# Kernel tuning notes

Hardware: AMD Instinct MI355X
Metric: run time of the kernel (lower is better)

## Reference

```python
import jax, jax.numpy as jnp
import numpy as np

S1, S2 = 8, 8          # support_size per hub
N, F, B = 100000, 128, 2048
EDGE_DIM = 1


def setup_inputs() -> dict:
    key = jax.random.key(0)
    ks = jax.random.split(key, 6)
    return {
        "features": jax.random.normal(ks[0], (N, F), dtype=jnp.float32),
        "in_sample_amnt": jax.random.uniform(ks[1], (N, S1, EDGE_DIM), dtype=jnp.float32),
        "out_sample_amnt": jax.random.uniform(ks[2], (N, S1, EDGE_DIM), dtype=jnp.float32),
        "in_sample": jax.random.randint(ks[3], (N, S1), 0, N),
        "out_sample": jax.random.randint(ks[4], (N, S1), 0, N),
        "node_ids": jax.random.randint(ks[5], (B,), 0, N),
    }


def _hop(features, sample, amnt, node_ids, support):
    """One hop of __get_next_hub: gather sampled neighbor ids, their edge
    weights, and [edge_weight || node_features] per neighbor."""
    nxt = sample[node_ids][..., :support]              # [..., support] int ids
    w = amnt[node_ids][..., :support, :]               # [..., support, EDGE_DIM]
    f = jnp.concatenate([w, features[nxt]], axis=-1)   # [..., support, EDGE_DIM+F]
    return nxt, f, w[..., 0]                           # squeeze first weight channel


def _branch(features, samples, amnts, node_ids, direction):
    """Hub-1 gather in `direction`, then hub-2 gathers in both directions,
    combined exactly as __get_input_layer does at hub == len(support_size)."""
    nn1, f1, w1 = _hop(features, samples[direction], amnts[direction], node_ids, S1)
    f1 = f1[..., None, :]                              # [B,S1,1,1+F]
    w1 = w1[..., None]                                 # [B,S1,1]
    _, f2i, w2i = _hop(features, samples["in"], amnts["in"], nn1, S2)    # [B,S1,S2,1+F]
    _, f2o, w2o = _hop(features, samples["out"], amnts["out"], nn1, S2)
    # concat([feat, next_in_feat, feat, next_out_feat], -2)
    feat = jnp.concatenate([f1, f2i, f1, f2o], axis=-2)  # [B,S1,2+2*S2,1+F]
    # weight loop collapses to one level (hub-1 weight has a single channel):
    # head = factor**2, deeper weights multiplied by the hub-1 factor.
    head = w1 ** 2
    wc = jnp.concatenate([head, w2i * w1, head, w2o * w1], axis=-1)  # [B,S1,2+2*S2]
    b = feat.shape[0]
    m = S1 * (2 + 2 * S2)
    return feat.reshape(b, m, feat.shape[-1]), wc.reshape(b, m)


def reference(features, in_sample_amnt, out_sample_amnt, in_sample, out_sample, node_ids):
    samples = {"in": in_sample, "out": out_sample}
    amnts = {"in": in_sample_amnt, "out": out_sample_amnt}
    fi, wi = _branch(features, samples, amnts, node_ids, "in")
    fo, wo = _branch(features, samples, amnts, node_ids, "out")
    feat = jnp.concatenate([fi, fo], axis=1)           # [B, 2*S1*(2+2*S2), 1+F]
    weight = jnp.concatenate([wi, wo], axis=1)         # [B, 2*S1*(2+2*S2)]
    # pack (feat, weight) into a single tensor: last channel is the weight
    return jnp.concatenate([feat, weight[..., None]], axis=-1)
```

## Files before the change

### kernel.cpp

```cpp
#include <hip/hip_runtime.h>

constexpr int S1 = 8, S2 = 8, F = 128;
constexpr int ROWS_PER_BRANCH = S1 * (2 + 2 * S2);
constexpr int ROWS_PER_B = 2 * ROWS_PER_BRANCH;
constexpr int ROW_LEN = F + 2;
constexpr int TOTAL_ROWS = 2048 * ROWS_PER_B;
constexpr int SLOTS = ROW_LEN / 2;
constexpr unsigned TOTAL_THREADS = 9360u * 256u;
constexpr int SLOTS_PER_THREAD = 16;

typedef float f32x2 __attribute__((ext_vector_type(2)));
typedef unsigned int u32;

__global__ __launch_bounds__(256) void gae_meta(
    const float* __restrict__ in_amnt,
    const float* __restrict__ out_amnt,
    const int*   __restrict__ in_sample,
    const int*   __restrict__ out_sample,
    const int*   __restrict__ node_ids,
    int4*        __restrict__ meta)
{
    const int row = blockIdx.x * blockDim.x + threadIdx.x;
    const int b  = row / ROWS_PER_B;
    const int r  = row - b * ROWS_PER_B;
    const int d1 = r / ROWS_PER_BRANCH;
    const int rr = r - d1 * ROWS_PER_BRANCH;
    const int s1 = rr / 18;
    const int lr = rr - s1 * 18;

    const int   nid = node_ids[b];
    const int   e1  = nid * S1 + s1;
    const int   n1  = d1 ? out_sample[e1] : in_sample[e1];
    const float w1  = d1 ? out_amnt[e1]   : in_amnt[e1];

    int node; float wf, wt;
    if (lr == 0 || lr == 9) {
        node = n1; wf = w1; wt = w1 * w1;
    } else if (lr <= 8) {
        const int e2 = n1 * S2 + (lr - 1);
        const float w2 = in_amnt[e2];
        node = in_sample[e2]; wf = w2; wt = w2 * w1;
    } else {
        const int e2 = n1 * S2 + (lr - 10);
        const float w2 = out_amnt[e2];
        node = out_sample[e2]; wf = w2; wt = w2 * w1;
    }

    int4 m;
    m.x = node;
    m.y = __float_as_int(wf);
    m.z = __float_as_int(wt);
    m.w = 0;
    meta[row] = m;
}

__global__ __launch_bounds__(256) void gae_scatter(
    const float* __restrict__ features,
    const int4*  __restrict__ meta,
    float*       __restrict__ out)
{
    const u32 tid = blockIdx.x * blockDim.x + threadIdx.x;
    f32x2* __restrict__ out2 = (f32x2*)out;

    #pragma unroll 4
    for (int k = 0; k < SLOTS_PER_THREAD; ++k) {
        const u32 s   = tid + (u32)k * TOTAL_THREADS;
        const u32 row = s / 65u;
        const u32 j   = s - row * 65u;

        const int4  m    = meta[row];
        const float wf   = __int_as_float(m.y);
        const float wt   = __int_as_float(m.z);
        const float* __restrict__ frow = features + (size_t)m.x * F;

        const u32 iA = (j == 0u)  ? 0u   : (2u * j - 1u);
        const u32 iB = (j >= 64u) ? 127u : (2u * j);
        const float a  = frow[iA];
        const float bv = frow[iB];

        f32x2 v;
        v.x = (j == 0u)  ? wf : a;
        v.y = (j == 64u) ? wt : bv;
        __builtin_nontemporal_store(v, &out2[s]);
    }
}

extern "C" void kernel_launch(void* const* d_in, const int* in_sizes, int n_in,
                              void* d_out, int out_size, void* d_ws, size_t ws_size,
                              hipStream_t stream) {
    const float* features   = (const float*)d_in[0];
    const float* in_amnt    = (const float*)d_in[1];
    const float* out_amnt   = (const float*)d_in[2];
    const int*   in_sample  = (const int*)d_in[3];
    const int*   out_sample = (const int*)d_in[4];
    const int*   node_ids   = (const int*)d_in[5];
    float*       out        = (float*)d_out;
    int4*        meta       = (int4*)d_ws;

    gae_meta<<<TOTAL_ROWS / 256, 256, 0, stream>>>(in_amnt, out_amnt,
                                                   in_sample, out_sample,
                                                   node_ids, meta);
    gae_scatter<<<9360, 256, 0, stream>>>(features, meta, out);
}
```

Measured before the change: 102.6 us.

## Sort output rows by source node via counting sort to improve gather locality

Adds a counting sort of output rows keyed by gathered node id: atomic histogram in the meta kernel, a three-kernel prefix scan, and a placement kernel that builds a row order. The scatter kernel then walks rows in node-sorted order, so rows that gather the same feature row run close together in time and should hit in cache. In exchange it adds five extra launches, a memset, global atomics, and output stores that are no longer contiguous across consecutive threads.

```diff
diff --git a/kernel.cpp b/kernel.cpp
--- a/kernel.cpp
+++ b/kernel.cpp
@@ -3,14 +3,20 @@
 constexpr int S1 = 8, S2 = 8, F = 128;
 constexpr int ROWS_PER_BRANCH = S1 * (2 + 2 * S2);
 constexpr int ROWS_PER_B = 2 * ROWS_PER_BRANCH;
-constexpr int ROW_LEN = F + 2;
 constexpr int TOTAL_ROWS = 2048 * ROWS_PER_B;
-constexpr int SLOTS = ROW_LEN / 2;
+constexpr int NNODES = 100000;
+constexpr int SCAN_BLK = 1024;
+constexpr int NBLK = (NNODES + SCAN_BLK - 1) / SCAN_BLK;
 constexpr unsigned TOTAL_THREADS = 9360u * 256u;
 constexpr int SLOTS_PER_THREAD = 16;
 
 typedef float f32x2 __attribute__((ext_vector_type(2)));
 typedef unsigned int u32;
+
+constexpr size_t OFF_NODEA = 9437184;
+constexpr size_t OFF_ORDER = 11796480;
+constexpr size_t OFF_BINS  = 14155776;
+constexpr size_t OFF_BSUM  = 14555776;
 
 __global__ __launch_bounds__(256) void gae_meta(
     const float* __restrict__ in_amnt,
@@ -18,7 +24,7 @@
     const int*   __restrict__ in_sample,
     const int*   __restrict__ out_sample,
     const int*   __restrict__ node_ids,
-    int4*        __restrict__ meta)
+    int4* __restrict__ meta, u32* __restrict__ nodeA, u32* __restrict__ bins)
 {
     const int row = blockIdx.x * blockDim.x + threadIdx.x;
     const int b  = row / ROWS_PER_B;
@@ -46,17 +52,60 @@
         node = out_sample[e2]; wf = w2; wt = w2 * w1;
     }
 
-    int4 m;
-    m.x = node;
-    m.y = __float_as_int(wf);
-    m.z = __float_as_int(wt);
-    m.w = 0;
-    meta[row] = m;
+    int4 m; m.x = node; m.y = __float_as_int(wf); m.z = __float_as_int(wt); m.w = 0;
+    meta[row]  = m;
+    nodeA[row] = (u32)node;
+    atomicAdd(&bins[node], 1u);
+}
+
+__global__ __launch_bounds__(SCAN_BLK) void scan1(u32* __restrict__ bins,
+                                                  u32* __restrict__ bsum)
+{
+    __shared__ u32 tmp[SCAN_BLK];
+    const int t = threadIdx.x;
+    const int i = blockIdx.x * SCAN_BLK + t;
+    const u32 c = (i < NNODES) ? bins[i] : 0u;
+    tmp[t] = c;
+    __syncthreads();
+    for (int off = 1; off < SCAN_BLK; off <<= 1) {
+        const u32 v = tmp[t];
+        const u32 a = (t >= off) ? tmp[t - off] : 0u;
+        __syncthreads();
+        tmp[t] = v + a;
+        __syncthreads();
+    }
+    if (i < NNODES) bins[i] = tmp[t] - c;
+    if (t == SCAN_BLK - 1) bsum[blockIdx.x] = tmp[t];
+}
+
+__global__ void scan2(u32* __restrict__ bsum)
+{
+    if (threadIdx.x == 0 && blockIdx.x == 0) {
+        u32 run = 0;
+        for (int b = 0; b < NBLK; ++b) { const u32 v = bsum[b]; bsum[b] = run; run += v; }
+    }
+}
+
+__global__ __launch_bounds__(SCAN_BLK) void scan3(u32* __restrict__ bins,
+                                                  const u32* __restrict__ bsum)
+{
+    const int i = blockIdx.x * SCAN_BLK + threadIdx.x;
+    if (i < NNODES) bins[i] += bsum[blockIdx.x];
+}
+
+__global__ __launch_bounds__(256) void gae_place(
+    const u32* __restrict__ nodeA, u32* __restrict__ bins, u32* __restrict__ order)
+{
+    const int row = blockIdx.x * blockDim.x + threadIdx.x;
+    const u32 node = nodeA[row];
+    const u32 pos  = atomicAdd(&bins[node], 1u);
+    order[pos] = (u32)row;
 }
 
 __global__ __launch_bounds__(256) void gae_scatter(
     const float* __restrict__ features,
     const int4*  __restrict__ meta,
+    const u32*   __restrict__ order,
     float*       __restrict__ out)
 {
     const u32 tid = blockIdx.x * blockDim.x + threadIdx.x;
@@ -65,12 +114,13 @@
     #pragma unroll 4
     for (int k = 0; k < SLOTS_PER_THREAD; ++k) {
         const u32 s   = tid + (u32)k * TOTAL_THREADS;
-        const u32 row = s / 65u;
-        const u32 j   = s - row * 65u;
+        const u32 kk  = s / 65u;
+        const u32 j   = s - kk * 65u;
+        const u32 row = order[kk];
 
-        const int4  m    = meta[row];
-        const float wf   = __int_as_float(m.y);
-        const float wt   = __int_as_float(m.z);
+        const int4  m  = meta[row];
+        const float wf = __int_as_float(m.y);
+        const float wt = __int_as_float(m.z);
         const float* __restrict__ frow = features + (size_t)m.x * F;
 
         const u32 iA = (j == 0u)  ? 0u   : (2u * j - 1u);
@@ -81,7 +131,7 @@
         f32x2 v;
         v.x = (j == 0u)  ? wf : a;
         v.y = (j == 64u) ? wt : bv;
-        __builtin_nontemporal_store(v, &out2[s]);
+        __builtin_nontemporal_store(v, &out2[(size_t)row * 65u + j]);
     }
 }
 
@@ -95,10 +145,21 @@
     const int*   out_sample = (const int*)d_in[4];
     const int*   node_ids   = (const int*)d_in[5];
     float*       out        = (float*)d_out;
-    int4*        meta       = (int4*)d_ws;
 
-    gae_meta<<<TOTAL_ROWS / 256, 256, 0, stream>>>(in_amnt, out_amnt,
-                                                   in_sample, out_sample,
-                                                   node_ids, meta);
-    gae_scatter<<<9360, 256, 0, stream>>>(features, meta, out);
+    char* ws    = (char*)d_ws;
+    int4* meta  = (int4*)ws;
+    u32*  nodeA = (u32*)(ws + OFF_NODEA);
+    u32*  order = (u32*)(ws + OFF_ORDER);
+    u32*  bins  = (u32*)(ws + OFF_BINS);
+    u32*  bsum  = (u32*)(ws + OFF_BSUM);
+
+    hipMemsetAsync(bins, 0, NNODES * sizeof(u32), stream);
+    gae_meta<<<TOTAL_ROWS / 256, 256, 0, stream>>>(in_amnt, out_amnt, in_sample,
+                                                   out_sample, node_ids,
+                                                   meta, nodeA, bins);
+    scan1<<<NBLK, SCAN_BLK, 0, stream>>>(bins, bsum);
+    scan2<<<1, 64, 0, stream>>>(bsum);
+    scan3<<<NBLK, SCAN_BLK, 0, stream>>>(bins, bsum);
+    gae_place<<<TOTAL_ROWS / 256, 256, 0, stream>>>(nodeA, bins, order);
+    gae_scatter<<<9360, 256, 0, stream>>>(features, meta, order, out);
 }
```

New measurement: 220.7 us. 2.15x slower.
